# Kernel tuning notes

Measured on AMD Instinct MI355X. Metric: run time of the kernel, lower is better.

Reference implementation:

```python
import jax, jax.numpy as jnp
import numpy as np

B, N, SEQ = 4, 1024, 512
FOUR = SEQ // 2 + 1           # 257, rfft output length
E = N * 32                    # edges from adjacency nonzeros
H1, C1 = 3, 10                # gat1: heads=3, out=10 (concat -> 30)
H2, C2 = 1, 1                 # gat2: heads=1, out=1
NEG_SLOPE = 0.2               # GATConv default negative_slope
PRE_L = 1


def setup_inputs() -> dict:
    ks = jax.random.split(jax.random.key(0), 14)
    occ = jax.random.normal(ks[0], (B, N, SEQ), dtype=jnp.float32)
    prc = jax.random.normal(ks[1], (B, N, SEQ), dtype=jnp.float32)
    # edge_index = adj_dense.nonzero().t(): indices in [0, N)
    edge_index = jax.random.randint(ks[2], (2, E), 0, N, dtype=jnp.int32)
    s = 0.3
    W1 = jax.random.normal(ks[3], (2, H1 * C1), dtype=jnp.float32) * s
    att_src1 = jax.random.normal(ks[4], (1, H1, C1), dtype=jnp.float32) * s
    att_dst1 = jax.random.normal(ks[5], (1, H1, C1), dtype=jnp.float32) * s
    b1 = jnp.zeros((H1 * C1,), dtype=jnp.float32)
    W2 = jax.random.normal(ks[6], (H1 * C1, H2 * C2), dtype=jnp.float32) * s
    att_src2 = jax.random.normal(ks[7], (1, H2, C2), dtype=jnp.float32) * s
    att_dst2 = jax.random.normal(ks[8], (1, H2, C2), dtype=jnp.float32) * s
    b2 = jnp.zeros((H2 * C2,), dtype=jnp.float32)
    dec_W = jax.random.normal(ks[9], (FOUR, PRE_L), dtype=jnp.float32) * (1.0 / np.sqrt(FOUR))
    dec_b = jnp.zeros((PRE_L,), dtype=jnp.float32)
    return {"occ": occ, "prc": prc, "edge_index": edge_index,
            "W1": W1, "att_src1": att_src1, "att_dst1": att_dst1, "b1": b1,
            "W2": W2, "att_src2": att_src2, "att_dst2": att_dst2, "b2": b2,
            "dec_W": dec_W, "dec_b": dec_b}


def gat_layer(x, src, dst, W, att_src, att_dst, bias, heads, ch):
    # x: [Nt, Fin]. PyG GATConv (concat=True, eval mode: no dropout).
    Nt = x.shape[0]
    h = (x @ W).reshape(Nt, heads, ch)                 # [Nt, H, C]
    a_src = jnp.sum(h * att_src, axis=-1)              # [Nt, H]
    a_dst = jnp.sum(h * att_dst, axis=-1)              # [Nt, H]
    e = jax.nn.leaky_relu(a_src[src] + a_dst[dst], NEG_SLOPE)  # [Ee, H]
    # segment softmax over destination nodes
    m = jax.ops.segment_max(e, dst, num_segments=Nt)   # [Nt, H]
    ex = jnp.exp(e - m[dst])
    denom = jax.ops.segment_sum(ex, dst, num_segments=Nt)
    alpha = ex / denom[dst]                            # [Ee, H]
    out = jax.ops.segment_sum(h[src] * alpha[..., None], dst, num_segments=Nt)
    return out.reshape(Nt, heads * ch) + bias


def reference(occ, prc, edge_index, W1, att_src1, att_dst1, b1,
              W2, att_src2, att_dst2, b2, dec_W, dec_b):
    # stack -> [B, N, SEQ, 2]; rfft over seq dim; keep real part
    x = jnp.stack([occ, prc], axis=-1)
    x = jnp.fft.rfft(x, axis=2).real                   # [B, N, FOUR, 2]
    x = x.reshape(-1, 2)                               # [Nt, 2], Nt = B*N*FOUR
    Nt = x.shape[0]
    # GATConv adds self-loops for every row of x (num_nodes = Nt)
    loops = jnp.arange(Nt, dtype=edge_index.dtype)
    src = jnp.concatenate([edge_index[0], loops])
    dst = jnp.concatenate([edge_index[1], loops])
    x = gat_layer(x, src, dst, W1, att_src1, att_dst1, b1, H1, C1)  # [Nt, 30]
    x = jax.nn.elu(x)
    x = gat_layer(x, src, dst, W2, att_src2, att_dst2, b2, H2, C2)  # [Nt, 1]
    # dropout is identity in eval mode
    x = x.reshape(B, N, FOUR)
    return x @ dec_W + dec_b                           # [B, N, PRE_L]
```

## Files before the change

kernel.cpp:

```cpp
#include <hip/hip_runtime.h>
#include <math.h>

constexpr int Bc    = 4;
constexpr int Nc    = 1024;
constexpr int SEQc  = 512;
constexpr int FOURc = 257;
constexpr int NROWS = Bc * Nc;
constexpr int NSMALL = 1024;
constexpr int F1c   = 30;
constexpr int CAP   = 128;
constexpr int XPAD  = 258;
constexpr float NEG_SLOPE = 0.2f;

#define DEVFN static __device__ __forceinline__

__global__ __launch_bounds__(256) void k_xf(
    const float* __restrict__ occ, const float* __restrict__ prc,
    float* __restrict__ xf, int* __restrict__ cnt) {
  __shared__ float4 z[2][128];
  __shared__ float sp[2][6];
  const int tid  = threadIdx.x;
  const int lane = tid & 63;
  const int wid  = tid >> 6;
  const int jrow = wid >> 1;
  const int half = wid & 1;
  const int row  = blockIdx.x * 2 + jrow;

  if (blockIdx.x == 0) {
#pragma unroll
    for (int j = 0; j < 4; ++j) cnt[tid + 256 * j] = 0;
  }

  {
    const int j = tid >> 7;
    const int t = tid & 127;
    const float* ro = occ + (size_t)(blockIdx.x * 2 + j) * SEQc;
    const float* rp = prc + (size_t)(blockIdx.x * 2 + j) * SEQc;
    if (t == 0) {
      sp[j][0] = ro[0];                 sp[j][1] = rp[0];
      sp[j][2] = ro[128] + ro[384];     sp[j][3] = rp[128] + rp[384];
      sp[j][4] = ro[256];               sp[j][5] = rp[256];
    } else {
      float ao = ro[t] + ro[SEQc - t];
      float bo = ro[256 - t] + ro[256 + t];
      float ap = rp[t] + rp[SEQc - t];
      float bp = rp[256 - t] + rp[256 + t];
      z[j][t] = make_float4(ao + bo, ap + bp, ao - bo, ap - bp);
    }
  }
  __syncthreads();

  const int k0 = half * 128 + 2 * lane;
  const float a = 6.283185307179586f / 512.0f;
  float ce = cosf((float)k0 * a),       cpe = 1.f, m2e = 2.f * ce;
  float co = cosf((float)(k0 + 1) * a), cpo = 1.f, m2o = 2.f * co;
  float aeo = 0.f, aep = 0.f, aoo = 0.f, aop = 0.f;

#pragma unroll 4
  for (int t = 1; t < 128; ++t) {
    float4 zv = z[jrow][t];
    aeo = fmaf(zv.x, ce, aeo);
    aep = fmaf(zv.y, ce, aep);
    aoo = fmaf(zv.z, co, aoo);
    aop = fmaf(zv.w, co, aop);
    float ne = fmaf(m2e, ce, -cpe); cpe = ce; ce = ne;
    float no = fmaf(m2o, co, -cpo); cpo = co; co = no;
  }

  const float y0o = sp[jrow][0], y0p = sp[jrow][1];
  const float y128o = sp[jrow][2], y128p = sp[jrow][3];
  const float x256o = sp[jrow][4], x256p = sp[jrow][5];
  const float s128 = (lane & 1) ? -1.f : 1.f;

  float4 st;
  st.x = aeo + y0o + s128 * y128o + x256o;
  st.y = aep + y0p + s128 * y128p + x256p;
  st.z = aoo + y0o - x256o;
  st.w = aop + y0p - x256p;
  *reinterpret_cast<float4*>(xf + ((size_t)row * XPAD + k0) * 2) = st;

  if (half == 0) {
    float sgn = (lane & 1) ? -1.f : 1.f;
    float4 zhi = z[jrow][lane + 64];
    float so = sgn * zhi.x, spp = sgn * zhi.y;
    if (lane >= 1) {
      float4 zlo = z[jrow][lane];
      so  = fmaf(sgn, zlo.x, so);
      spp = fmaf(sgn, zlo.y, spp);
    }
#pragma unroll
    for (int off = 32; off; off >>= 1) {
      so  += __shfl_xor(so, off);
      spp += __shfl_xor(spp, off);
    }
    if (lane == 0) {
      float2 st2;
      st2.x = y0o + y128o + so + x256o;
      st2.y = y0p + y128p + spp + x256p;
      *reinterpret_cast<float2*>(xf + ((size_t)row * XPAD + 256) * 2) = st2;
    }
  }
}

__global__ __launch_bounds__(256) void k_pre(const int* __restrict__ ei, int E,
                                             int* __restrict__ cnt,
                                             int* __restrict__ srcs2) {
  const int base = blockIdx.x * 256 + threadIdx.x;
  const int tot  = E + NSMALL;
  for (int e = base; e < tot; e += 32 * 256) {
    int src, dst;
    if (e < E) { src = ei[e]; dst = ei[E + e]; }
    else       { src = dst = e - E; }
    int pos = atomicAdd(&cnt[dst], 1);
    if (pos < CAP) srcs2[dst * CAP + pos] = src;
  }
}

DEVFN float node_v(float xo, float xp,
                   const float* w1s, const float* b1s, const float* w2s, float b2v) {
  float s = 0.f;
#pragma unroll
  for (int jj = 0; jj < F1c; ++jj) {
    float h = fmaf(xo, w1s[jj], fmaf(xp, w1s[F1c + jj], b1s[jj]));
    float e = h > 0.f ? h : (__expf(h) - 1.f);
    s = fmaf(e, w2s[jj], s);
  }
  return s + b2v;
}

DEVFN void small_prep(int node, float xo, float xp,
                      const float* w1s, const float* s1, const float* d1,
                      float* h1s, float* a1s, float* a1d) {
#pragma unroll
  for (int h = 0; h < 3; ++h) {
    float as = 0.f, ad = 0.f;
#pragma unroll
    for (int c = 0; c < 10; ++c) {
      int jj = h * 10 + c;
      float hv = fmaf(xo, w1s[jj], xp * w1s[F1c + jj]);
      h1s[node * F1c + jj] = hv;
      as = fmaf(hv, s1[jj], as);
      ad = fmaf(hv, d1[jj], ad);
    }
    a1s[node * 3 + h] = as;
    a1d[node * 3 + h] = ad;
  }
}

__global__ __launch_bounds__(256) void k_post(
    const float* __restrict__ xf,
    const float* __restrict__ W1, const float* __restrict__ b1,
    const float* __restrict__ W2, const float* __restrict__ b2,
    const float* __restrict__ as1, const float* __restrict__ ad1,
    const float* __restrict__ decW, const float* __restrict__ decb,
    float* __restrict__ out, float* __restrict__ vsm,
    float* __restrict__ h1s, float* __restrict__ a1s, float* __restrict__ a1d) {
  __shared__ float wl[192];
  __shared__ float red[4];
  const int tid = threadIdx.x;
  const int row = blockIdx.x;
  if      (tid < 60)  wl[tid] = W1[tid];
  else if (tid < 90)  wl[tid] = b1[tid - 60];
  else if (tid < 120) wl[tid] = W2[tid - 90];
  else if (tid < 150) wl[tid] = as1[tid - 120];
  else if (tid < 180) wl[tid] = ad1[tid - 150];
  __syncthreads();
  const float* w1s = wl;
  const float* b1s = wl + 60;
  const float* w2s = wl + 90;
  const float* s1  = wl + 120;
  const float* d1  = wl + 150;
  const float b2v  = b2[0];
  const bool smallrow = (row < 4);

  float2 v2 = *reinterpret_cast<const float2*>(xf + ((size_t)row * XPAD + tid) * 2);
  float vv = node_v(v2.x, v2.y, w1s, b1s, w2s, b2v);
  float s = vv * decW[tid];
  if (tid == 0) {
    float2 v6 = *reinterpret_cast<const float2*>(xf + ((size_t)row * XPAD + 256) * 2);
    float v256 = node_v(v6.x, v6.y, w1s, b1s, w2s, b2v);
    s = fmaf(v256, decW[256], s);
    if (smallrow) {
      int node = row * FOURc + 256;
      if (node < NSMALL) {
        vsm[node] = v256;
        small_prep(node, v6.x, v6.y, w1s, s1, d1, h1s, a1s, a1d);
      }
    }
  }
  if (smallrow) {
    int node = row * FOURc + tid;
    if (node < NSMALL) {
      vsm[node] = vv;
      small_prep(node, v2.x, v2.y, w1s, s1, d1, h1s, a1s, a1d);
    }
  }
#pragma unroll
  for (int off = 32; off; off >>= 1) s += __shfl_xor(s, off);
  if ((tid & 63) == 0) red[tid >> 6] = s;
  __syncthreads();
  if (tid == 0) out[row] = red[0] + red[1] + red[2] + red[3] + decb[0];
}

__global__ __launch_bounds__(256) void k_g1(
    const int* __restrict__ cnt, const int* __restrict__ srcs2,
    const float* __restrict__ a1s, const float* __restrict__ a1d,
    const float* __restrict__ h1s,
    const float* __restrict__ b1, const float* __restrict__ W2,
    const float* __restrict__ as2, const float* __restrict__ ad2,
    float* __restrict__ h2s, float* __restrict__ a2s, float* __restrict__ a2d) {
  const int lane = threadIdx.x & 63;
  const int dst  = blockIdx.x * 4 + (threadIdx.x >> 6);
  const int deg  = cnt[dst];
  const int* sp  = srcs2 + dst * CAP;
  const float ad0 = a1d[dst * 3], ad1v = a1d[dst * 3 + 1], ad2v = a1d[dst * 3 + 2];
  float den[3] = {0.f, 0.f, 0.f};
  float num[F1c];
#pragma unroll
  for (int j = 0; j < F1c; ++j) num[j] = 0.f;

  for (int p = lane; p < deg; p += 64) {
    int src = sp[p];
    const float* hs = h1s + src * F1c;
    float x0 = a1s[src * 3]     + ad0;
    float x1 = a1s[src * 3 + 1] + ad1v;
    float x2 = a1s[src * 3 + 2] + ad2v;
    x0 = x0 > 0.f ? x0 : NEG_SLOPE * x0;
    x1 = x1 > 0.f ? x1 : NEG_SLOPE * x1;
    x2 = x2 > 0.f ? x2 : NEG_SLOPE * x2;
    float e0 = __expf(x0), e1 = __expf(x1), e2 = __expf(x2);
    den[0] += e0; den[1] += e1; den[2] += e2;
#pragma unroll
    for (int c = 0; c < 10; ++c) {
      num[c]      = fmaf(e0, hs[c],      num[c]);
      num[10 + c] = fmaf(e1, hs[10 + c], num[10 + c]);
      num[20 + c] = fmaf(e2, hs[20 + c], num[20 + c]);
    }
  }
#pragma unroll
  for (int h = 0; h < 3; ++h)
#pragma unroll
    for (int off = 32; off; off >>= 1) den[h] += __shfl_xor(den[h], off);
#pragma unroll
  for (int j = 0; j < F1c; ++j)
#pragma unroll
    for (int off = 32; off; off >>= 1) num[j] += __shfl_xor(num[j], off);

  if (lane == 0) {
    float h2 = 0.f;
#pragma unroll
    for (int jj = 0; jj < F1c; ++jj) {
      float x2 = num[jj] / den[jj / 10] + b1[jj];
      x2 = x2 > 0.f ? x2 : (__expf(x2) - 1.f);
      h2 = fmaf(x2, W2[jj], h2);
    }
    h2s[dst] = h2;
    a2s[dst] = h2 * as2[0];
    a2d[dst] = h2 * ad2[0];
  }
}

__global__ __launch_bounds__(256) void k_g2(
    const int* __restrict__ cnt, const int* __restrict__ srcs2,
    const float* __restrict__ a2s, const float* __restrict__ a2d,
    const float* __restrict__ h2s, const float* __restrict__ b2,
    const float* __restrict__ vsm, const float* __restrict__ decW,
    float* __restrict__ out) {
  __shared__ float rcor[4];
  __shared__ int   rrow[4];
  const int tid  = threadIdx.x;
  const int lane = tid & 63;
  const int wid  = tid >> 6;
  const int dst  = blockIdx.x * 4 + wid;
  const int deg  = cnt[dst];
  const int* sp  = srcs2 + dst * CAP;
  const float adv = a2d[dst];
  float den = 0.f, num = 0.f;
  for (int p = lane; p < deg; p += 64) {
    int src = sp[p];
    float x = a2s[src] + adv;
    x = x > 0.f ? x : NEG_SLOPE * x;
    float ex = __expf(x);
    den += ex;
    num = fmaf(ex, h2s[src], num);
  }
#pragma unroll
  for (int off = 32; off; off >>= 1) {
    den += __shfl_xor(den, off);
    num += __shfl_xor(num, off);
  }
  if (lane == 0) {
    float val2v = num / den + b2[0];
    int r = dst / FOURc;
    int k = dst - r * FOURc;
    rcor[wid] = (val2v - vsm[dst]) * decW[k];
    rrow[wid] = r;
  }
  __syncthreads();
  if (tid == 0) {
    float acc = rcor[0];
#pragma unroll
    for (int i = 1; i < 4; ++i) {
      if (rrow[i] == rrow[0]) acc += rcor[i];
      else atomicAdd(&out[rrow[i]], rcor[i]);
    }
    atomicAdd(&out[rrow[0]], acc);
  }
}

extern "C" void kernel_launch(void* const* d_in, const int* in_sizes, int n_in,
                              void* d_out, int out_size, void* d_ws, size_t ws_size,
                              hipStream_t stream) {
  const float* occ  = (const float*)d_in[0];
  const float* prc  = (const float*)d_in[1];
  const int*   ei   = (const int*)d_in[2];
  const float* W1   = (const float*)d_in[3];
  const float* as1  = (const float*)d_in[4];
  const float* ad1  = (const float*)d_in[5];
  const float* b1   = (const float*)d_in[6];
  const float* W2   = (const float*)d_in[7];
  const float* as2  = (const float*)d_in[8];
  const float* ad2  = (const float*)d_in[9];
  const float* b2   = (const float*)d_in[10];
  const float* decW = (const float*)d_in[11];
  const float* decb = (const float*)d_in[12];
  const int E = in_sizes[2] / 2;

  float* ws = (float*)d_ws;
  float* xf   = ws;
  float* h1s  = xf + (size_t)NROWS * XPAD * 2;
  float* a1s  = h1s + NSMALL * F1c;
  float* a1d  = a1s + NSMALL * 3;
  float* h2s  = a1d + NSMALL * 3;
  float* a2s  = h2s + NSMALL;
  float* a2d  = a2s + NSMALL;
  float* vsm  = a2d + NSMALL;
  int*   cnt  = (int*)(vsm + NSMALL);
  int*   srcs2 = cnt + NSMALL;

  k_xf<<<NROWS / 2, 256, 0, stream>>>(occ, prc, xf, cnt);

  k_pre<<<32, 256, 0, stream>>>(ei, E, cnt, srcs2);

  k_post<<<NROWS, 256, 0, stream>>>(xf, W1, b1, W2, b2, as1, ad1,
                                    decW, decb, (float*)d_out, vsm,
                                    h1s, a1s, a1d);

  k_g1<<<NSMALL / 4, 256, 0, stream>>>(cnt, srcs2, a1s, a1d, h1s,
                                       b1, W2, as2, ad2, h2s, a2s, a2d);
  k_g2<<<NSMALL / 4, 256, 0, stream>>>(cnt, srcs2, a2s, a2d, h2s, b2,
                                       vsm, decW, (float*)d_out);
}
```

Baseline: 57.81 us.

## Fold edge bucketing into k_post and pad node features for vector loads

The separate edge-bucketing kernel is removed, and its work now runs in 32 extra blocks appended to the k_post launch. This saves one kernel launch and lets the bucketing overlap with the per-row post-processing. The small-node feature arrays are padded to strides of 32 and 4 so the gather loop in k_g1 can use float4 and float2 loads. The padding adds some workspace, and the extra blocks make k_post branch on block index.

Measured after the change: 54.16 us, median of 3. 6.3% less time.

```diff
diff --git a/kernel.cpp b/kernel.cpp
--- a/kernel.cpp
+++ b/kernel.cpp
@@ -8,6 +8,7 @@
 constexpr int NROWS = Bc * Nc;
 constexpr int NSMALL = 1024;
 constexpr int F1c   = 30;
+constexpr int PADH  = 32;
 constexpr int CAP   = 128;
 constexpr int XPAD  = 258;
 constexpr float NEG_SLOPE = 0.2f;
@@ -102,20 +103,6 @@
   }
 }
 
-__global__ __launch_bounds__(256) void k_pre(const int* __restrict__ ei, int E,
-                                             int* __restrict__ cnt,
-                                             int* __restrict__ srcs2) {
-  const int base = blockIdx.x * 256 + threadIdx.x;
-  const int tot  = E + NSMALL;
-  for (int e = base; e < tot; e += 32 * 256) {
-    int src, dst;
-    if (e < E) { src = ei[e]; dst = ei[E + e]; }
-    else       { src = dst = e - E; }
-    int pos = atomicAdd(&cnt[dst], 1);
-    if (pos < CAP) srcs2[dst * CAP + pos] = src;
-  }
-}
-
 DEVFN float node_v(float xo, float xp,
                    const float* w1s, const float* b1s, const float* w2s, float b2v) {
   float s = 0.f;
@@ -138,12 +125,12 @@
     for (int c = 0; c < 10; ++c) {
       int jj = h * 10 + c;
       float hv = fmaf(xo, w1s[jj], xp * w1s[F1c + jj]);
-      h1s[node * F1c + jj] = hv;
+      h1s[node * PADH + jj] = hv;
       as = fmaf(hv, s1[jj], as);
       ad = fmaf(hv, d1[jj], ad);
     }
-    a1s[node * 3 + h] = as;
-    a1d[node * 3 + h] = ad;
+    a1s[node * 4 + h] = as;
+    a1d[node * 4 + h] = ad;
   }
 }
 
@@ -154,10 +141,26 @@
     const float* __restrict__ as1, const float* __restrict__ ad1,
     const float* __restrict__ decW, const float* __restrict__ decb,
     float* __restrict__ out, float* __restrict__ vsm,
-    float* __restrict__ h1s, float* __restrict__ a1s, float* __restrict__ a1d) {
+    float* __restrict__ h1s, float* __restrict__ a1s, float* __restrict__ a1d,
+    const int* __restrict__ ei, int E,
+    int* __restrict__ cnt, int* __restrict__ srcs2) {
+  const int tid = threadIdx.x;
+
+  if (blockIdx.x >= NROWS) {
+    const int base = (blockIdx.x - NROWS) * 256 + tid;
+    const int tot  = E + NSMALL;
+    for (int e = base; e < tot; e += 32 * 256) {
+      int src, dst;
+      if (e < E) { src = ei[e]; dst = ei[E + e]; }
+      else       { src = dst = e - E; }
+      int pos = atomicAdd(&cnt[dst], 1);
+      if (pos < CAP) srcs2[dst * CAP + pos] = src;
+    }
+    return;
+  }
+
   __shared__ float wl[192];
   __shared__ float red[4];
-  const int tid = threadIdx.x;
   const int row = blockIdx.x;
   if      (tid < 60)  wl[tid] = W1[tid];
   else if (tid < 90)  wl[tid] = b1[tid - 60];
@@ -213,7 +216,7 @@
   const int dst  = blockIdx.x * 4 + (threadIdx.x >> 6);
   const int deg  = cnt[dst];
   const int* sp  = srcs2 + dst * CAP;
-  const float ad0 = a1d[dst * 3], ad1v = a1d[dst * 3 + 1], ad2v = a1d[dst * 3 + 2];
+  const float ad0 = a1d[dst * 4], ad1v = a1d[dst * 4 + 1], ad2v = a1d[dst * 4 + 2];
   float den[3] = {0.f, 0.f, 0.f};
   float num[F1c];
 #pragma unroll
@@ -221,21 +224,27 @@
 
   for (int p = lane; p < deg; p += 64) {
     int src = sp[p];
-    const float* hs = h1s + src * F1c;
-    float x0 = a1s[src * 3]     + ad0;
-    float x1 = a1s[src * 3 + 1] + ad1v;
-    float x2 = a1s[src * 3 + 2] + ad2v;
+    const float4* hs4 = reinterpret_cast<const float4*>(h1s + src * PADH);
+    float4 av = *reinterpret_cast<const float4*>(a1s + src * 4);
+    float x0 = av.x + ad0;
+    float x1 = av.y + ad1v;
+    float x2 = av.z + ad2v;
     x0 = x0 > 0.f ? x0 : NEG_SLOPE * x0;
     x1 = x1 > 0.f ? x1 : NEG_SLOPE * x1;
     x2 = x2 > 0.f ? x2 : NEG_SLOPE * x2;
-    float e0 = __expf(x0), e1 = __expf(x1), e2 = __expf(x2);
-    den[0] += e0; den[1] += e1; den[2] += e2;
-#pragma unroll
-    for (int c = 0; c < 10; ++c) {
-      num[c]      = fmaf(e0, hs[c],      num[c]);
-      num[10 + c] = fmaf(e1, hs[10 + c], num[10 + c]);
-      num[20 + c] = fmaf(e2, hs[20 + c], num[20 + c]);
-    }
+    float ev[3] = {__expf(x0), __expf(x1), __expf(x2)};
+    den[0] += ev[0]; den[1] += ev[1]; den[2] += ev[2];
+#pragma unroll
+    for (int m = 0; m < 7; ++m) {
+      float4 hv = hs4[m];
+      num[4 * m + 0] = fmaf(ev[(4 * m + 0) / 10], hv.x, num[4 * m + 0]);
+      num[4 * m + 1] = fmaf(ev[(4 * m + 1) / 10], hv.y, num[4 * m + 1]);
+      num[4 * m + 2] = fmaf(ev[(4 * m + 2) / 10], hv.z, num[4 * m + 2]);
+      num[4 * m + 3] = fmaf(ev[(4 * m + 3) / 10], hv.w, num[4 * m + 3]);
+    }
+    float2 h7 = *reinterpret_cast<const float2*>(h1s + src * PADH + 28);
+    num[28] = fmaf(ev[2], h7.x, num[28]);
+    num[29] = fmaf(ev[2], h7.y, num[29]);
   }
 #pragma unroll
   for (int h = 0; h < 3; ++h)
@@ -329,9 +338,9 @@
   float* ws = (float*)d_ws;
   float* xf   = ws;
   float* h1s  = xf + (size_t)NROWS * XPAD * 2;
-  float* a1s  = h1s + NSMALL * F1c;
-  float* a1d  = a1s + NSMALL * 3;
-  float* h2s  = a1d + NSMALL * 3;
+  float* a1s  = h1s + NSMALL * PADH;
+  float* a1d  = a1s + NSMALL * 4;
+  float* h2s  = a1d + NSMALL * 4;
   float* a2s  = h2s + NSMALL;
   float* a2d  = a2s + NSMALL;
   float* vsm  = a2d + NSMALL;
@@ -340,11 +349,9 @@
 
   k_xf<<<NROWS / 2, 256, 0, stream>>>(occ, prc, xf, cnt);
 
-  k_pre<<<32, 256, 0, stream>>>(ei, E, cnt, srcs2);
-
-  k_post<<<NROWS, 256, 0, stream>>>(xf, W1, b1, W2, b2, as1, ad1,
-                                    decW, decb, (float*)d_out, vsm,
-                                    h1s, a1s, a1d);
+  k_post<<<NROWS + 32, 256, 0, stream>>>(xf, W1, b1, W2, b2, as1, ad1,
+                                         decW, decb, (float*)d_out, vsm,
+                                         h1s, a1s, a1d, ei, E, cnt, srcs2);
 
   k_g1<<<NSMALL / 4, 256, 0, stream>>>(cnt, srcs2, a1s, a1d, h1s,
                                        b1, W2, as2, ad2, h2s, a2s, a2d);
```
